# Optimization experiments

Hardware: AMD Instinct MI355X
Metric: run time of the kernel (lower is better)

The kernel has to match this reference:

```python
import jax, jax.numpy as jnp
import numpy as np

N_POS = 10  # number of child positions encoded in U_f (10*h_size rows)


def setup_inputs() -> dict:
    key = jax.random.key(0)
    ks = jax.random.split(key, 12)
    N, H = 32768, 128
    s = 0.05  # keep activations in a sane range
    return {
        "child_h": jax.random.normal(ks[0], (N, 1, H), jnp.float32),
        "child_c": jax.random.normal(ks[1], (N, 1, H), jnp.float32),
        "extra_input_depth_1": jax.random.normal(ks[2], (N, H), jnp.float32),
        "extra_input_depth_2": jax.random.normal(ks[3], (N, H), jnp.float32),
        "h_prev": jax.random.normal(ks[4], (N, H), jnp.float32),
        "pos": jax.random.randint(ks[5], (N,), 0, N_POS, jnp.int32),
        "depth": jax.random.randint(ks[6], (N,), 0, 4, jnp.int32),
        "mask": jax.random.randint(ks[7], (N,), 0, 2, jnp.int32),
        "W_f": jax.random.normal(ks[8], (N_POS * H, H), jnp.float32) * s,
        "b_f": jax.random.normal(ks[9], (N_POS * H,), jnp.float32) * s,
        "W_iou": jax.random.normal(ks[10], (3 * H, N_POS * H), jnp.float32) * s,
        "b_iou": jax.random.normal(ks[11], (1, 3 * H), jnp.float32) * s,
    }


def reference(child_h, child_c, extra_input_depth_1, extra_input_depth_2,
              h_prev, pos, depth, mask, W_f, b_f, W_iou, b_iou):
    N, _, H = child_h.shape
    dt = child_h.dtype
    # reduce_func: flatten mailbox (single child => last_dim == h_size)
    h_cat = child_h.reshape(N, H)
    # masked injection of extra inputs by depth
    h_cat = h_cat + extra_input_depth_2 * (depth == 2).astype(dt)[:, None]
    h_cat = h_cat + extra_input_depth_1 * (depth == 1).astype(dt)[:, None]
    # per-position grouped matmuls against weight slices, scattered back by pos mask
    W_f_r = W_f.reshape(N_POS, H, H)          # row slice pos*H:(pos+1)*H
    b_f_r = b_f.reshape(N_POS, H)
    W_iou_r = W_iou.reshape(3 * H, N_POS, H)  # col slice pos*H:(pos+1)*H
    u = jnp.zeros((N, H), dt)
    iou = jnp.zeros((N, 3 * H), dt)
    for p in range(N_POS):  # small fixed group count
        sel = (pos == p)[:, None]
        u = jnp.where(sel, h_cat @ W_f_r[p] + b_f_r[p][None, :], u)
        iou = jnp.where(sel, h_cat @ W_iou_r[:, p, :].T, iou)
    # sigmoid forget gate, children-sum of cell states
    f = jax.nn.sigmoid(u)
    c_red = jnp.sum(f[:, None, :] * child_c, axis=1)  # [N, H]
    # apply_node_func
    iou = iou + b_iou
    i, o, uu = jnp.split(iou, 3, axis=1)
    c_new = jax.nn.sigmoid(i) * jnp.tanh(uu) + c_red
    h_new = jax.nn.sigmoid(o) * jnp.tanh(c_new)
    # update_masked_nodes=False: blend (note: DGL node 'c' was overwritten by reduce)
    m = mask.astype(dt)[:, None]
    h = h_prev * m + (1.0 - m) * h_new
    c = c_red * m + (1.0 - m) * c_new
    return h, c
```

## Files before the change

kernel.cpp:

```cpp
#include <hip/hip_runtime.h>

#define H 128
#define NPOS 10
#define ROWSB 32
#define BLOCK 512

using bf16x8 = __attribute__((ext_vector_type(8))) short;
using f32x4  = __attribute__((ext_vector_type(4))) float;

__device__ __forceinline__ unsigned short f2bf(float f) {
  unsigned u = __float_as_uint(f);
  u += 0x7FFFu + ((u >> 16) & 1u);
  return (unsigned short)(u >> 16);
}

__device__ __forceinline__ float sigm(float x) {
  return __builtin_amdgcn_rcpf(1.0f + __builtin_amdgcn_exp2f(-1.44269504f * x));
}
__device__ __forceinline__ float tanh_f(float x) {
  return 2.0f * __builtin_amdgcn_rcpf(1.0f + __builtin_amdgcn_exp2f(-2.88539008f * x)) - 1.0f;
}

__global__ void prep_wt(const float* __restrict__ Wf, const float* __restrict__ Wiou,
                        unsigned short* __restrict__ wt,
                        const int* __restrict__ posp, int* __restrict__ hist2,
                        int N, int nhb) {
  int b = blockIdx.x, t = threadIdx.x;
  if (b < NPOS * 16) {
    __shared__ float tile[32][33];
    int p = b >> 4, jt = (b >> 2) & 3, kt = b & 3;
    int tx = t & 31, ty = t >> 5;
    #pragma unroll
    for (int it = 0; it < 4; ++it) {
      int krow = kt * 32 + ty + it * 8;
      int j = jt * 32 + tx;
      tile[ty + it * 8][tx] = Wf[(size_t)(p * H + krow) * H + j];
    }
    __syncthreads();
    #pragma unroll
    for (int it = 0; it < 4; ++it) {
      int j2 = jt * 32 + ty + it * 8;
      int k2 = kt * 32 + tx;
      wt[(size_t)p * 512 * H + (size_t)j2 * H + k2] = f2bf(tile[tx][ty + it * 8]);
    }
  } else if (b < NPOS * 16 + (NPOS * 384 * H) / 256) {
    int id = (b - NPOS * 16) * 256 + t;
    int p = id / 49152;
    int r = id - p * 49152;
    int k = r & 127;
    float v = Wiou[(size_t)(r >> 7) * (NPOS * H) + p * H + k];
    wt[(size_t)p * 65536 + 16384 + r] = f2bf(v);
  } else {
    int hb = b - (NPOS * 16 + (NPOS * 384 * H) / 256);
    __shared__ int c[NPOS];
    if (t < NPOS) c[t] = 0;
    __syncthreads();
    int i = hb * 256 + t;
    if (i < N) atomicAdd(&c[posp[i]], 1);
    __syncthreads();
    if (t < NPOS) hist2[hb * 16 + t] = c[t];
  }
}

__global__ void scan_build(const int* __restrict__ hist2, int nhb,
                           int* __restrict__ off2,
                           int* __restrict__ blkpos, int* __restrict__ blkgs,
                           int* __restrict__ blkcnt, int maxb) {
  __shared__ int tot[NPOS], base[NPOS + 1], bb[NPOS + 1];
  int t = threadIdx.x;
  int w = t >> 6, l = t & 63;
  if (w < NPOS) {
    int b0 = 2 * l, b1 = 2 * l + 1;
    int a  = (b0 < nhb) ? hist2[b0 * 16 + w] : 0;
    int bv = (b1 < nhb) ? hist2[b1 * 16 + w] : 0;
    int s = a + bv, sc = s;
    #pragma unroll
    for (int off = 1; off < 64; off <<= 1) {
      int u = __shfl_up(sc, off);
      if (l >= off) sc += u;
    }
    int excl = sc - s;
    if (b0 < nhb) off2[b0 * 16 + w] = excl;
    if (b1 < nhb) off2[b1 * 16 + w] = excl + a;
    if (l == 63) tot[w] = sc;
  }
  __syncthreads();
  if (t == 0) {
    int run = 0, rb = 0;
    for (int p = 0; p < NPOS; ++p) {
      base[p] = run; bb[p] = rb;
      run += tot[p];
      rb += (tot[p] + ROWSB - 1) / ROWSB;
    }
    base[NPOS] = run; bb[NPOS] = rb;
  }
  __syncthreads();
  for (int i = t; i < nhb * NPOS; i += 640) {
    int b = i / NPOS, p = i - b * NPOS;
    off2[b * 16 + p] += base[p];
  }
  int nb = bb[NPOS];
  for (int b = t; b < maxb; b += 640) {
    if (b < nb) {
      int p = 0;
      while (bb[p + 1] <= b) ++p;
      int s = (b - bb[p]) * ROWSB;
      blkpos[b] = p;
      blkgs[b] = base[p] + s;
      blkcnt[b] = min(ROWSB, tot[p] - s);
    } else {
      blkpos[b] = -1;
    }
  }
}

__global__ void scatter_idx(const int* __restrict__ posp, const int* __restrict__ depthp,
                            const int* __restrict__ maskp, const int* __restrict__ off2,
                            unsigned* __restrict__ order, int N) {
  __shared__ int c[NPOS], basearr[NPOS];
  int hb = blockIdx.x, t = threadIdx.x;
  if (t < NPOS) { c[t] = 0; basearr[t] = off2[hb * 16 + t]; }
  __syncthreads();
  int i = hb * 256 + t;
  int p = -1, r = 0;
  unsigned e = 0;
  if (i < N) {
    p = posp[i];
    r = atomicAdd(&c[p], 1);
    int d = depthp[i];
    int mk = maskp[i];
    e = (unsigned)i | ((unsigned)mk << 16) |
        ((unsigned)(d == 1) << 17) | ((unsigned)(d == 2) << 18);
  }
  __syncthreads();
  if (p >= 0) order[basearr[p] + r] = e;
}

__global__ __launch_bounds__(BLOCK, 3) void tree_lstm_main(
    const float* __restrict__ child_h, const float* __restrict__ child_c,
    const float* __restrict__ e1, const float* __restrict__ e2,
    const float* __restrict__ h_prev,
    const float* __restrict__ b_f, const float* __restrict__ b_iou,
    const unsigned short* __restrict__ wt,
    const unsigned* __restrict__ order, const int* __restrict__ blkpos,
    const int* __restrict__ blkgs, const int* __restrict__ blkcnt,
    float* __restrict__ out, int N) {

  const int b = blockIdx.x;
  const int p = blkpos[b];
  if (p < 0) return;
  const int gs = blkgs[b], cnth = blkcnt[b];

  __shared__ unsigned short hs[ROWSB * H];
  __shared__ unsigned rowg[ROWSB];

  const int t = threadIdx.x;
  const int wv = t >> 6, l = t & 63;
  const int l15 = l & 15, lhi = l >> 4;
  const int colr = wv * 16 + l15;
  const int kof = lhi * 8;

  const unsigned short* wb0 = wt + (size_t)p * 512 * H + (size_t)colr * H + kof;

  if (t < ROWSB) rowg[t] = (t < cnth) ? order[gs + t] : 0xFFFFFFFFu;
  __syncthreads();

  {
    int id = t;
    int row = id >> 4, c8 = id & 15;
    unsigned e = rowg[row];
    float4 a0 = {0.f, 0.f, 0.f, 0.f}, a1 = {0.f, 0.f, 0.f, 0.f};
    if ((int)e >= 0) {
      int g = e & 0xFFFF;
      const float4* ph = (const float4*)(child_h + (size_t)g * H + c8 * 8);
      a0 = ph[0]; a1 = ph[1];
      if (e & (3u << 17)) {
        const float* ep = (e & (1u << 17)) ? e1 : e2;
        const float4* pe = (const float4*)(ep + (size_t)g * H + c8 * 8);
        float4 b0 = pe[0], b1 = pe[1];
        a0.x += b0.x; a0.y += b0.y; a0.z += b0.z; a0.w += b0.w;
        a1.x += b1.x; a1.y += b1.y; a1.z += b1.z; a1.w += b1.w;
      }
    }
    bf16x8 v;
    v[0] = (short)f2bf(a0.x); v[1] = (short)f2bf(a0.y);
    v[2] = (short)f2bf(a0.z); v[3] = (short)f2bf(a0.w);
    v[4] = (short)f2bf(a1.x); v[5] = (short)f2bf(a1.y);
    v[6] = (short)f2bf(a1.z); v[7] = (short)f2bf(a1.w);
    int wb = (row * 256 + c8 * 16) ^ ((row & 7) << 4);
    *(bf16x8*)((char*)hs + wb) = v;
  }
  __syncthreads();

  const size_t NH = (size_t)N * H;
  const float bfv = b_f[p * H + colr];
  const float b_i = b_iou[colr], b_o = b_iou[H + colr], b_g = b_iou[2 * H + colr];

  const int nchunk = (cnth + 15) >> 4;
  for (int c = 0; c < nchunk; ++c) {
    const int r0 = c * 16;

    bf16x8 Bu[4], Biq[4], Boq[4], Bgq[4];
    #pragma unroll
    for (int kk = 0; kk < 4; ++kk) {
      Bu[kk]  = *(const bf16x8*)(wb0 + kk * 32);
      Biq[kk] = *(const bf16x8*)(wb0 + 128 * H + kk * 32);
      Boq[kk] = *(const bf16x8*)(wb0 + 256 * H + kk * 32);
      Bgq[kk] = *(const bf16x8*)(wb0 + 384 * H + kk * 32);
    }
    __builtin_amdgcn_sched_barrier(0);

    unsigned gg[4]; float cc[4], hpv[4];
    #pragma unroll
    for (int q = 0; q < 4; ++q) {
      int rr = r0 + lhi * 4 + q;
      gg[q] = (rr < cnth) ? rowg[rr] : 0xFFFFFFFFu;
    }
    #pragma unroll
    for (int q = 0; q < 4; ++q) {
      if ((int)gg[q] >= 0) {
        size_t gi = (size_t)(gg[q] & 0xFFFF) * H + colr;
        cc[q] = child_c[gi];
        hpv[q] = h_prev[gi];
      } else { cc[q] = 0.f; hpv[q] = 0.f; }
    }
    __builtin_amdgcn_sched_barrier(0);

    const int arow = r0 + l15;
    bf16x8 afr[4];
    #pragma unroll
    for (int kk = 0; kk < 4; ++kk) {
      int rb = (arow * 256 + kk * 64 + lhi * 16) ^ ((arow & 7) << 4);
      afr[kk] = *(const bf16x8*)((const char*)hs + rb);
    }

    f32x4 au = {0.f, 0.f, 0.f, 0.f};
    f32x4 ai = {0.f, 0.f, 0.f, 0.f};
    f32x4 ao = {0.f, 0.f, 0.f, 0.f};
    f32x4 ag = {0.f, 0.f, 0.f, 0.f};
    #pragma unroll
    for (int kk = 0; kk < 4; ++kk) {
      au = __builtin_amdgcn_mfma_f32_16x16x32_bf16(afr[kk], Bu[kk],  au, 0, 0, 0);
      ai = __builtin_amdgcn_mfma_f32_16x16x32_bf16(afr[kk], Biq[kk], ai, 0, 0, 0);
      ao = __builtin_amdgcn_mfma_f32_16x16x32_bf16(afr[kk], Boq[kk], ao, 0, 0, 0);
      ag = __builtin_amdgcn_mfma_f32_16x16x32_bf16(afr[kk], Bgq[kk], ag, 0, 0, 0);
    }

    #pragma unroll
    for (int q = 0; q < 4; ++q) {
      if ((int)gg[q] >= 0) {
        size_t gi = (size_t)(gg[q] & 0xFFFF) * H + colr;
        float u = au[q] + bfv;
        float iv = ai[q] + b_i;
        float ov = ao[q] + b_o;
        float gv = ag[q] + b_g;
        float f = sigm(u);
        float credv = f * cc[q];
        float cnew = sigm(iv) * tanh_f(gv) + credv;
        float hnew = sigm(ov) * tanh_f(cnew);
        float m = (float)((gg[q] >> 16) & 1u);
        float hv = hpv[q] * m + (1.0f - m) * hnew;
        float cv = credv * m + (1.0f - m) * cnew;
        out[gi] = hv;
        out[NH + gi] = cv;
      }
    }
  }
}

extern "C" void kernel_launch(void* const* d_in, const int* in_sizes, int n_in,
                              void* d_out, int out_size, void* d_ws, size_t ws_size,
                              hipStream_t stream) {
  const float* child_h = (const float*)d_in[0];
  const float* child_c = (const float*)d_in[1];
  const float* e1      = (const float*)d_in[2];
  const float* e2      = (const float*)d_in[3];
  const float* h_prev  = (const float*)d_in[4];
  const int*   posp    = (const int*)d_in[5];
  const int*   depthp  = (const int*)d_in[6];
  const int*   maskp   = (const int*)d_in[7];
  const float* W_f     = (const float*)d_in[8];
  const float* b_f     = (const float*)d_in[9];
  const float* W_iou   = (const float*)d_in[10];
  const float* b_iou   = (const float*)d_in[11];
  float* out = (float*)d_out;
  int N = in_sizes[0] / H;
  int nhb = (N + 255) / 256;
  int maxb = NPOS + N / ROWSB;

  unsigned short* wt = (unsigned short*)d_ws;
  int* hist2  = (int*)((char*)d_ws + (size_t)NPOS * 512 * H * 2);
  int* off2   = hist2 + nhb * 16;
  int* blkpos = off2 + nhb * 16;
  int* blkgs  = blkpos + maxb;
  int* blkcnt = blkgs + maxb;
  unsigned* order = (unsigned*)(blkcnt + maxb);

  int prep_blocks = NPOS * 16 + (NPOS * 384 * H) / 256 + nhb;
  hipLaunchKernelGGL(prep_wt, dim3(prep_blocks), dim3(256), 0, stream,
                     W_f, W_iou, wt, posp, hist2, N, nhb);
  hipLaunchKernelGGL(scan_build, dim3(1), dim3(640), 0, stream,
                     hist2, nhb, off2, blkpos, blkgs, blkcnt, maxb);
  hipLaunchKernelGGL(scatter_idx, dim3(nhb), dim3(256), 0, stream,
                     posp, depthp, maskp, off2, order, N);
  hipLaunchKernelGGL(tree_lstm_main, dim3(maxb), dim3(BLOCK), 0, stream,
                     child_h, child_c, e1, e2, h_prev,
                     b_f, b_iou, wt, order, blkpos, blkgs, blkcnt, out, N);
}
```

Baseline: 49.97 us.

## Split GEMM and gate epilogue into separate kernels via bf16 gate buffer

When workspace allows, the main kernel writes bf16 pre-activation gates into a sorted-order buffer instead of gathering child_c/h_prev and scattering outputs. A new epilogue kernel reads the gates through a rank map and applies the LSTM nonlinearities with coalesced row-order loads and nontemporal stores. This aims to replace scattered per-row gathers and stores with contiguous access. The cost is an extra launch, an extra round trip of a 32 MB gate buffer through memory, and bf16 rounding of the pre-activations.

```diff
diff --git a/kernel.cpp b/kernel.cpp
--- a/kernel.cpp
+++ b/kernel.cpp
@@ -13,7 +13,9 @@
   u += 0x7FFFu + ((u >> 16) & 1u);
   return (unsigned short)(u >> 16);
 }
-
+__device__ __forceinline__ float bf2f(unsigned short s) {
+  return __uint_as_float(((unsigned)s) << 16);
+}
 __device__ __forceinline__ float sigm(float x) {
   return __builtin_amdgcn_rcpf(1.0f + __builtin_amdgcn_exp2f(-1.44269504f * x));
 }
@@ -116,7 +118,7 @@
 
 __global__ void scatter_idx(const int* __restrict__ posp, const int* __restrict__ depthp,
                             const int* __restrict__ maskp, const int* __restrict__ off2,
-                            unsigned* __restrict__ order, int N) {
+                            unsigned* __restrict__ order, int* __restrict__ rank, int N) {
   __shared__ int c[NPOS], basearr[NPOS];
   int hb = blockIdx.x, t = threadIdx.x;
   if (t < NPOS) { c[t] = 0; basearr[t] = off2[hb * 16 + t]; }
@@ -133,9 +135,14 @@
         ((unsigned)(d == 1) << 17) | ((unsigned)(d == 2) << 18);
   }
   __syncthreads();
-  if (p >= 0) order[basearr[p] + r] = e;
-}
-
+  if (p >= 0) {
+    int s = basearr[p] + r;
+    order[s] = e;
+    rank[i] = s;
+  }
+}
+
+template <int MODE>
 __global__ __launch_bounds__(BLOCK, 3) void tree_lstm_main(
     const float* __restrict__ child_h, const float* __restrict__ child_c,
     const float* __restrict__ e1, const float* __restrict__ e2,
@@ -144,7 +151,7 @@
     const unsigned short* __restrict__ wt,
     const unsigned* __restrict__ order, const int* __restrict__ blkpos,
     const int* __restrict__ blkgs, const int* __restrict__ blkcnt,
-    float* __restrict__ out, int N) {
+    unsigned short* __restrict__ gates, float* __restrict__ out, int N) {
 
   const int b = blockIdx.x;
   const int p = blkpos[b];
@@ -166,8 +173,7 @@
   __syncthreads();
 
   {
-    int id = t;
-    int row = id >> 4, c8 = id & 15;
+    int row = t >> 4, c8 = t & 15;
     unsigned e = rowg[row];
     float4 a0 = {0.f, 0.f, 0.f, 0.f}, a1 = {0.f, 0.f, 0.f, 0.f};
     if ((int)e >= 0) {
@@ -208,23 +214,23 @@
       Boq[kk] = *(const bf16x8*)(wb0 + 256 * H + kk * 32);
       Bgq[kk] = *(const bf16x8*)(wb0 + 384 * H + kk * 32);
     }
-    __builtin_amdgcn_sched_barrier(0);
 
     unsigned gg[4]; float cc[4], hpv[4];
-    #pragma unroll
-    for (int q = 0; q < 4; ++q) {
-      int rr = r0 + lhi * 4 + q;
-      gg[q] = (rr < cnth) ? rowg[rr] : 0xFFFFFFFFu;
-    }
-    #pragma unroll
-    for (int q = 0; q < 4; ++q) {
-      if ((int)gg[q] >= 0) {
-        size_t gi = (size_t)(gg[q] & 0xFFFF) * H + colr;
-        cc[q] = child_c[gi];
-        hpv[q] = h_prev[gi];
-      } else { cc[q] = 0.f; hpv[q] = 0.f; }
-    }
-    __builtin_amdgcn_sched_barrier(0);
+    if (MODE == 0) {
+      #pragma unroll
+      for (int q = 0; q < 4; ++q) {
+        int rr = r0 + lhi * 4 + q;
+        gg[q] = (rr < cnth) ? rowg[rr] : 0xFFFFFFFFu;
+      }
+      #pragma unroll
+      for (int q = 0; q < 4; ++q) {
+        if ((int)gg[q] >= 0) {
+          size_t gi = (size_t)(gg[q] & 0xFFFF) * H + colr;
+          cc[q] = child_c[gi];
+          hpv[q] = h_prev[gi];
+        } else { cc[q] = 0.f; hpv[q] = 0.f; }
+      }
+    }
 
     const int arow = r0 + l15;
     bf16x8 afr[4];
@@ -248,23 +254,63 @@
 
     #pragma unroll
     for (int q = 0; q < 4; ++q) {
-      if ((int)gg[q] >= 0) {
-        size_t gi = (size_t)(gg[q] & 0xFFFF) * H + colr;
-        float u = au[q] + bfv;
-        float iv = ai[q] + b_i;
-        float ov = ao[q] + b_o;
-        float gv = ag[q] + b_g;
-        float f = sigm(u);
-        float credv = f * cc[q];
-        float cnew = sigm(iv) * tanh_f(gv) + credv;
-        float hnew = sigm(ov) * tanh_f(cnew);
-        float m = (float)((gg[q] >> 16) & 1u);
-        float hv = hpv[q] * m + (1.0f - m) * hnew;
-        float cv = credv * m + (1.0f - m) * cnew;
-        out[gi] = hv;
-        out[NH + gi] = cv;
+      int rr = r0 + lhi * 4 + q;
+      if (MODE == 1) {
+        if (rr < cnth) {
+          ushort4 gvv;
+          gvv.x = f2bf(au[q] + bfv);
+          gvv.y = f2bf(ai[q] + b_i);
+          gvv.z = f2bf(ao[q] + b_o);
+          gvv.w = f2bf(ag[q] + b_g);
+          *(ushort4*)(gates + (size_t)(gs + rr) * 512 + colr * 4) = gvv;
+        }
+      } else {
+        if ((int)gg[q] >= 0) {
+          size_t gi = (size_t)(gg[q] & 0xFFFF) * H + colr;
+          float u = au[q] + bfv;
+          float iv = ai[q] + b_i;
+          float ov = ao[q] + b_o;
+          float gv = ag[q] + b_g;
+          float f = sigm(u);
+          float credv = f * cc[q];
+          float cnew = sigm(iv) * tanh_f(gv) + credv;
+          float hnew = sigm(ov) * tanh_f(cnew);
+          float m = (float)((gg[q] >> 16) & 1u);
+          float hv = hpv[q] * m + (1.0f - m) * hnew;
+          float cv = credv * m + (1.0f - m) * cnew;
+          out[gi] = hv;
+          out[NH + gi] = cv;
+        }
       }
     }
+  }
+}
+
+__global__ __launch_bounds__(512) void epilogue_k(
+    const unsigned short* __restrict__ gates, const int* __restrict__ rank,
+    const float* __restrict__ child_c, const float* __restrict__ h_prev,
+    const int* __restrict__ maskp, float* __restrict__ out, int N) {
+  const int t = threadIdx.x;
+  const int col = t & 127;
+  const size_t NH = (size_t)N * H;
+  #pragma unroll
+  for (int it = 0; it < 4; ++it) {
+    int i = blockIdx.x * 16 + it * 4 + (t >> 7);
+    int r = rank[i];
+    float m = (float)maskp[i];
+    ushort4 gvv = *(const ushort4*)(gates + (size_t)r * 512 + col * 4);
+    size_t gi = (size_t)i * H + col;
+    float cc = child_c[gi];
+    float hp = h_prev[gi];
+    float u = bf2f(gvv.x), iv = bf2f(gvv.y), ov = bf2f(gvv.z), gv = bf2f(gvv.w);
+    float f = sigm(u);
+    float credv = f * cc;
+    float cnew = sigm(iv) * tanh_f(gv) + credv;
+    float hnew = sigm(ov) * tanh_f(cnew);
+    float hv = hp * m + (1.0f - m) * hnew;
+    float cv = credv * m + (1.0f - m) * cnew;
+    __builtin_nontemporal_store(hv, &out[gi]);
+    __builtin_nontemporal_store(cv, &out[NH + gi]);
   }
 }
 
@@ -288,13 +334,24 @@
   int nhb = (N + 255) / 256;
   int maxb = NPOS + N / ROWSB;
 
+  const size_t wt_bytes    = (size_t)NPOS * 512 * H * 2;
+  const size_t gates_bytes = (size_t)N * 512;
+  const size_t gates_b     = (size_t)N * 1024;
+  const size_t table_b     = (size_t)(nhb * 32 + maxb * 3 + 16) * 4 + (size_t)N * 8;
+
+  bool split = ws_size >= wt_bytes + gates_b + table_b + 1024;
+
   unsigned short* wt = (unsigned short*)d_ws;
-  int* hist2  = (int*)((char*)d_ws + (size_t)NPOS * 512 * H * 2);
+  char* cur = (char*)d_ws + wt_bytes;
+  unsigned short* gates = nullptr;
+  if (split) { gates = (unsigned short*)cur; cur += gates_b; }
+  int* hist2  = (int*)cur;
   int* off2   = hist2 + nhb * 16;
   int* blkpos = off2 + nhb * 16;
   int* blkgs  = blkpos + maxb;
   int* blkcnt = blkgs + maxb;
   unsigned* order = (unsigned*)(blkcnt + maxb);
+  int* rank = (int*)(order + N);
 
   int prep_blocks = NPOS * 16 + (NPOS * 384 * H) / 256 + nhb;
   hipLaunchKernelGGL(prep_wt, dim3(prep_blocks), dim3(256), 0, stream,
@@ -302,8 +359,16 @@
   hipLaunchKernelGGL(scan_build, dim3(1), dim3(640), 0, stream,
                      hist2, nhb, off2, blkpos, blkgs, blkcnt, maxb);
   hipLaunchKernelGGL(scatter_idx, dim3(nhb), dim3(256), 0, stream,
-                     posp, depthp, maskp, off2, order, N);
-  hipLaunchKernelGGL(tree_lstm_main, dim3(maxb), dim3(BLOCK), 0, stream,
-                     child_h, child_c, e1, e2, h_prev,
-                     b_f, b_iou, wt, order, blkpos, blkgs, blkcnt, out, N);
-}
+                     posp, depthp, maskp, off2, order, rank, N);
+  if (split) {
+    hipLaunchKernelGGL((tree_lstm_main<1>), dim3(maxb), dim3(BLOCK), 0, stream,
+                       child_h, child_c, e1, e2, h_prev,
+                       b_f, b_iou, wt, order, blkpos, blkgs, blkcnt, gates, out, N);
+    hipLaunchKernelGGL(epilogue_k, dim3(N / 16), dim3(512), 0, stream,
+                       gates, rank, child_c, h_prev, maskp, out, N);
+  } else {
+    hipLaunchKernelGGL((tree_lstm_main<0>), dim3(maxb), dim3(BLOCK), 0, stream,
+                       child_h, child_c, e1, e2, h_prev,
+                       b_f, b_iou, wt, order, blkpos, blkgs, blkcnt, gates, out, N);
+  }
+}
```

Measured after the change: 63.19 us. 26.4% more time.

## Stage per-position weights in LDS with MFMA-friendly layout, process both row chunks together

Applied to the files above, without the earlier changes.

The weight-prep kernel now writes the bf16 weights in a k-block-major interleaved layout. The main kernel copies each 32-wide k slice of the weights into shared memory with coalesced 16-byte loads, then reads B fragments from LDS. Previously each chunk of 16 rows re-read the B fragments straight from global memory with strided per-lane loads. Both 16-row chunks are now accumulated in one pass, and child_c/h_prev are prefetched before the GEMM. This trades extra barriers and 32KB of LDS per block, which may lower occupancy, for better weight-load coalescing and reuse.

```diff
diff --git a/kernel.cpp b/kernel.cpp
--- a/kernel.cpp
+++ b/kernel.cpp
@@ -13,7 +13,6 @@
   u += 0x7FFFu + ((u >> 16) & 1u);
   return (unsigned short)(u >> 16);
 }
-
 __device__ __forceinline__ float sigm(float x) {
   return __builtin_amdgcn_rcpf(1.0f + __builtin_amdgcn_exp2f(-1.44269504f * x));
 }
@@ -41,15 +40,18 @@
     for (int it = 0; it < 4; ++it) {
       int j2 = jt * 32 + ty + it * 8;
       int k2 = kt * 32 + tx;
-      wt[(size_t)p * 512 * H + (size_t)j2 * H + k2] = f2bf(tile[tx][ty + it * 8]);
+      size_t dst = (((size_t)(p * 4 + kt) * 4 + (tx >> 3)) * 512 + j2) * 8 + (tx & 7);
+      wt[dst] = f2bf(tile[tx][ty + it * 8]);
     }
   } else if (b < NPOS * 16 + (NPOS * 384 * H) / 256) {
     int id = (b - NPOS * 16) * 256 + t;
     int p = id / 49152;
     int r = id - p * 49152;
+    int j = 128 + (r >> 7);
     int k = r & 127;
     float v = Wiou[(size_t)(r >> 7) * (NPOS * H) + p * H + k];
-    wt[(size_t)p * 65536 + 16384 + r] = f2bf(v);
+    size_t dst = (((size_t)(p * 4 + (k >> 5)) * 4 + ((k >> 3) & 3)) * 512 + j) * 8 + (k & 7);
+    wt[dst] = f2bf(v);
   } else {
     int hb = b - (NPOS * 16 + (NPOS * 384 * H) / 256);
     __shared__ int c[NPOS];
@@ -152,22 +154,19 @@
   const int gs = blkgs[b], cnth = blkcnt[b];
 
   __shared__ unsigned short hs[ROWSB * H];
+  __shared__ unsigned short Bs[4 * 512 * 8];
   __shared__ unsigned rowg[ROWSB];
 
   const int t = threadIdx.x;
   const int wv = t >> 6, l = t & 63;
   const int l15 = l & 15, lhi = l >> 4;
   const int colr = wv * 16 + l15;
-  const int kof = lhi * 8;
-
-  const unsigned short* wb0 = wt + (size_t)p * 512 * H + (size_t)colr * H + kof;
 
   if (t < ROWSB) rowg[t] = (t < cnth) ? order[gs + t] : 0xFFFFFFFFu;
   __syncthreads();
 
   {
-    int id = t;
-    int row = id >> 4, c8 = id & 15;
+    int row = t >> 4, c8 = t & 15;
     unsigned e = rowg[row];
     float4 a0 = {0.f, 0.f, 0.f, 0.f}, a1 = {0.f, 0.f, 0.f, 0.f};
     if ((int)e >= 0) {
@@ -190,82 +189,78 @@
     int wb = (row * 256 + c8 * 16) ^ ((row & 7) << 4);
     *(bf16x8*)((char*)hs + wb) = v;
   }
-  __syncthreads();
+
+  unsigned gg[2][4]; float cc[2][4], hpv[2][4];
+  #pragma unroll
+  for (int c = 0; c < 2; ++c)
+    #pragma unroll
+    for (int q = 0; q < 4; ++q) {
+      int rr = c * 16 + lhi * 4 + q;
+      unsigned e = (rr < cnth) ? rowg[rr] : 0xFFFFFFFFu;
+      gg[c][q] = e;
+      if ((int)e >= 0) {
+        size_t gi = (size_t)(e & 0xFFFF) * H + colr;
+        cc[c][q] = child_c[gi];
+        hpv[c][q] = h_prev[gi];
+      } else { cc[c][q] = 0.f; hpv[c][q] = 0.f; }
+    }
+
+  __syncthreads();
+
+  f32x4 acc[2][4] = {};
+  const unsigned short* wtp = wt + (size_t)p * 65536;
+
+  #pragma unroll
+  for (int kk = 0; kk < 4; ++kk) {
+    if (kk) __syncthreads();
+    #pragma unroll
+    for (int i = 0; i < 4; ++i) {
+      int eo = (i * BLOCK + t) * 8;
+      *(bf16x8*)(Bs + eo) = *(const bf16x8*)(wtp + kk * 16384 + eo);
+    }
+    __syncthreads();
+
+    bf16x8 bfr[4];
+    #pragma unroll
+    for (int g4 = 0; g4 < 4; ++g4)
+      bfr[g4] = *(const bf16x8*)(Bs + ((lhi * 512) + (g4 * 128 + colr)) * 8);
+
+    #pragma unroll
+    for (int c = 0; c < 2; ++c) {
+      const int arow = c * 16 + l15;
+      int rb = (arow * 256 + kk * 64 + lhi * 16) ^ ((arow & 7) << 4);
+      bf16x8 afr = *(const bf16x8*)((const char*)hs + rb);
+      #pragma unroll
+      for (int g4 = 0; g4 < 4; ++g4)
+        acc[c][g4] = __builtin_amdgcn_mfma_f32_16x16x32_bf16(afr, bfr[g4], acc[c][g4], 0, 0, 0);
+    }
+  }
 
   const size_t NH = (size_t)N * H;
   const float bfv = b_f[p * H + colr];
   const float b_i = b_iou[colr], b_o = b_iou[H + colr], b_g = b_iou[2 * H + colr];
 
-  const int nchunk = (cnth + 15) >> 4;
-  for (int c = 0; c < nchunk; ++c) {
-    const int r0 = c * 16;
-
-    bf16x8 Bu[4], Biq[4], Boq[4], Bgq[4];
-    #pragma unroll
-    for (int kk = 0; kk < 4; ++kk) {
-      Bu[kk]  = *(const bf16x8*)(wb0 + kk * 32);
-      Biq[kk] = *(const bf16x8*)(wb0 + 128 * H + kk * 32);
-      Boq[kk] = *(const bf16x8*)(wb0 + 256 * H + kk * 32);
-      Bgq[kk] = *(const bf16x8*)(wb0 + 384 * H + kk * 32);
-    }
-    __builtin_amdgcn_sched_barrier(0);
-
-    unsigned gg[4]; float cc[4], hpv[4];
+  #pragma unroll
+  for (int c = 0; c < 2; ++c)
     #pragma unroll
     for (int q = 0; q < 4; ++q) {
-      int rr = r0 + lhi * 4 + q;
-      gg[q] = (rr < cnth) ? rowg[rr] : 0xFFFFFFFFu;
-    }
-    #pragma unroll
-    for (int q = 0; q < 4; ++q) {
-      if ((int)gg[q] >= 0) {
-        size_t gi = (size_t)(gg[q] & 0xFFFF) * H + colr;
-        cc[q] = child_c[gi];
-        hpv[q] = h_prev[gi];
-      } else { cc[q] = 0.f; hpv[q] = 0.f; }
-    }
-    __builtin_amdgcn_sched_barrier(0);
-
-    const int arow = r0 + l15;
-    bf16x8 afr[4];
-    #pragma unroll
-    for (int kk = 0; kk < 4; ++kk) {
-      int rb = (arow * 256 + kk * 64 + lhi * 16) ^ ((arow & 7) << 4);
-      afr[kk] = *(const bf16x8*)((const char*)hs + rb);
-    }
-
-    f32x4 au = {0.f, 0.f, 0.f, 0.f};
-    f32x4 ai = {0.f, 0.f, 0.f, 0.f};
-    f32x4 ao = {0.f, 0.f, 0.f, 0.f};
-    f32x4 ag = {0.f, 0.f, 0.f, 0.f};
-    #pragma unroll
-    for (int kk = 0; kk < 4; ++kk) {
-      au = __builtin_amdgcn_mfma_f32_16x16x32_bf16(afr[kk], Bu[kk],  au, 0, 0, 0);
-      ai = __builtin_amdgcn_mfma_f32_16x16x32_bf16(afr[kk], Biq[kk], ai, 0, 0, 0);
-      ao = __builtin_amdgcn_mfma_f32_16x16x32_bf16(afr[kk], Boq[kk], ao, 0, 0, 0);
-      ag = __builtin_amdgcn_mfma_f32_16x16x32_bf16(afr[kk], Bgq[kk], ag, 0, 0, 0);
-    }
-
-    #pragma unroll
-    for (int q = 0; q < 4; ++q) {
-      if ((int)gg[q] >= 0) {
-        size_t gi = (size_t)(gg[q] & 0xFFFF) * H + colr;
-        float u = au[q] + bfv;
-        float iv = ai[q] + b_i;
-        float ov = ao[q] + b_o;
-        float gv = ag[q] + b_g;
+      if ((int)gg[c][q] >= 0) {
+        size_t gi = (size_t)(gg[c][q] & 0xFFFF) * H + colr;
+        float u  = acc[c][0][q] + bfv;
+        float iv = acc[c][1][q] + b_i;
+        float ov = acc[c][2][q] + b_o;
+        float gv = acc[c][3][q] + b_g;
         float f = sigm(u);
-        float credv = f * cc[q];
+        float credv = f * cc[c][q];
         float cnew = sigm(iv) * tanh_f(gv) + credv;
         float hnew = sigm(ov) * tanh_f(cnew);
-        float m = (float)((gg[q] >> 16) & 1u);
-        float hv = hpv[q] * m + (1.0f - m) * hnew;
+        float m = (float)((gg[c][q] >> 16) & 1u);
+        float hv = hpv[c][q] * m + (1.0f - m) * hnew;
         float cv = credv * m + (1.0f - m) * cnew;
         out[gi] = hv;
         out[NH + gi] = cv;
       }
     }
-  }
 }
 
 extern "C" void kernel_launch(void* const* d_in, const int* in_sizes, int n_in,
```

Result: faster. 47.24 us (-5.5%).
